# Optimization experiments

Hardware: AMD Instinct MI355X
Metric: run time of the kernel (lower is better)

## Reference

```python
import jax, jax.numpy as jnp
import numpy as np


def setup_inputs() -> dict:
    key = jax.random.key(0)
    k1, k2, k3 = jax.random.split(key, 3)
    B, T, J, D = 32, 1024, 256, 512
    context = jax.random.normal(k1, (B, T, D), dtype=jnp.float32)
    query = jax.random.normal(k2, (B, J, D), dtype=jnp.float32)
    # nn.Linear(3*D, 1, bias=False) weight, flattened to (3D,)
    w_alpha = jax.random.normal(k3, (3 * D,), dtype=jnp.float32) * (1.0 / np.sqrt(3 * D))
    return {"context": context, "query": query, "w_alpha": w_alpha}


def reference(context, query, w_alpha):
    # context: [B,T,D], query: [B,J,D], w_alpha: [3D]
    D = context.shape[-1]
    w1, w2, w3 = w_alpha[:D], w_alpha[D:2 * D], w_alpha[2 * D:]
    # Decomposed trilinear score: S[b,t,j] = c_t.w1 + q_j.w2 + sum_d c_td q_jd w3_d
    # (identical math to expand+concat+Linear, without the B*T*J*3D intermediate)
    S = (context @ w1)[:, :, None] \
        + (query @ w2)[:, None, :] \
        + jnp.einsum('btd,bjd->btj', context * w3, query)  # [B,T,J]
    S_softmax_row = jax.nn.softmax(S, axis=1)              # softmax over context dim (as in source)
    b_t = jax.nn.softmax(jnp.max(S, axis=2), axis=1)       # [B,T]
    U_attd = jnp.einsum('btj,bjd->btd', S_softmax_row, query)  # [B,T,D]
    h = jnp.einsum('bt,btd->bd', b_t, context)             # [B,D]
    H_attd = h[:, None, :]                                  # broadcast over T
    G = jnp.concatenate(
        [context, U_attd, context * U_attd, context * H_attd], axis=2)  # [B,T,4D]
    return G
```

## Files before the change

kernel.cpp:

```cpp
#include <hip/hip_runtime.h>
#include <cmath>

constexpr int B = 32, T = 1024, J = 256, D = 512;

typedef __attribute__((ext_vector_type(8))) short bf16x8;
typedef __attribute__((ext_vector_type(4))) float f32x4;
typedef __attribute__((ext_vector_type(8))) unsigned short u16x8;
typedef __attribute__((ext_vector_type(4))) unsigned short u16x4;
using u16 = unsigned short;

constexpr size_t OFF_S   = 0;
constexpr size_t OFF_CH  = OFF_S   + (size_t)B*T*J;
constexpr size_t OFF_CL  = OFF_CH  + (size_t)B*T*D/2;
constexpr size_t OFF_QPH = OFF_CL  + (size_t)B*T*D/2;
constexpr size_t OFF_QPL = OFF_QPH + (size_t)B*J*D/2;
constexpr size_t OFF_QTH = OFF_QPL + (size_t)B*J*D/2;
constexpr size_t OFF_QTL = OFF_QTH + (size_t)B*J*D/2;
constexpr size_t OFF_PH  = OFF_QTL + (size_t)B*J*D/2;
constexpr size_t OFF_PLO = OFF_PH  + (size_t)B*T*J/2;
constexpr size_t OFF_RT  = OFF_PLO + (size_t)B*T*J/2;
constexpr size_t OFF_CT  = OFF_RT  + (size_t)B*T;
constexpr size_t OFF_M   = OFF_CT  + (size_t)B*J;
constexpr size_t OFF_IL  = OFF_M   + (size_t)B*J;
constexpr size_t OFF_RM  = OFF_IL  + (size_t)B*J;
constexpr size_t OFF_BT  = OFF_RM  + (size_t)B*T;
constexpr size_t OFF_H   = OFF_BT  + (size_t)B*T;
constexpr size_t OFF_PM  = OFF_H   + (size_t)B*D;
constexpr size_t OFF_PL2 = OFF_PM  + (size_t)B*16*J;

__device__ __forceinline__ u16 f2bf(float x) {
  unsigned u = __float_as_uint(x);
  u += 0x7FFFu + ((u >> 16) & 1u);
  return (u16)(u >> 16);
}
__device__ __forceinline__ float bf2f(u16 h) {
  return __uint_as_float((unsigned)h << 16);
}

__global__ void k_prep_c(const float* __restrict__ ctx, const float* __restrict__ w_alpha,
                         float* __restrict__ rt, u16* __restrict__ ch, u16* __restrict__ cl) {
  int wid = threadIdx.x >> 6, lane = threadIdx.x & 63;
  size_t row = (size_t)blockIdx.x * 4 + wid;
  const float4* s4 = (const float4*)(ctx + row * D);
  const float4* w4 = (const float4*)w_alpha;
  float4 a0 = s4[lane*2], a1 = s4[lane*2+1];
  float4 b0 = w4[lane*2], b1 = w4[lane*2+1];
  float acc = a0.x*b0.x + a0.y*b0.y + a0.z*b0.z + a0.w*b0.w
            + a1.x*b1.x + a1.y*b1.y + a1.z*b1.z + a1.w*b1.w;
  float v[8] = {a0.x,a0.y,a0.z,a0.w,a1.x,a1.y,a1.z,a1.w};
  u16x8 hv, lv;
  #pragma unroll
  for (int i = 0; i < 8; ++i) {
    u16 hb = f2bf(v[i]);
    hv[i] = hb;
    lv[i] = f2bf(v[i] - bf2f(hb));
  }
  *(u16x8*)(ch + row*D + lane*8) = hv;
  *(u16x8*)(cl + row*D + lane*8) = lv;
  #pragma unroll
  for (int off = 32; off; off >>= 1) acc += __shfl_down(acc, off);
  if (lane == 0) rt[row] = acc;
}

__global__ void k_prep_q(const float* __restrict__ q, const float* __restrict__ w_alpha,
                         float* __restrict__ ct, u16* __restrict__ qph, u16* __restrict__ qpl) {
  int wid = threadIdx.x >> 6, lane = threadIdx.x & 63;
  size_t row = (size_t)blockIdx.x * 4 + wid;
  const float4* q4 = (const float4*)(q + row * D);
  const float4* w2 = (const float4*)(w_alpha + D);
  const float4* w3 = (const float4*)(w_alpha + 2 * D);
  float4 a0 = q4[lane*2], a1 = q4[lane*2+1];
  float4 b0 = w2[lane*2], b1 = w2[lane*2+1];
  float4 c0 = w3[lane*2], c1 = w3[lane*2+1];
  float acc = a0.x*b0.x + a0.y*b0.y + a0.z*b0.z + a0.w*b0.w
            + a1.x*b1.x + a1.y*b1.y + a1.z*b1.z + a1.w*b1.w;
  float v[8] = {a0.x*c0.x, a0.y*c0.y, a0.z*c0.z, a0.w*c0.w,
                a1.x*c1.x, a1.y*c1.y, a1.z*c1.z, a1.w*c1.w};
  u16x8 hv, lv;
  #pragma unroll
  for (int i = 0; i < 8; ++i) {
    u16 hb = f2bf(v[i]);
    hv[i] = hb;
    lv[i] = f2bf(v[i] - bf2f(hb));
  }
  *(u16x8*)(qph + row*D + lane*8) = hv;
  *(u16x8*)(qpl + row*D + lane*8) = lv;
  #pragma unroll
  for (int off = 32; off; off >>= 1) acc += __shfl_down(acc, off);
  if (lane == 0) ct[row] = acc;
}

__global__ void k_qt(const float* __restrict__ q, u16* __restrict__ qth, u16* __restrict__ qtl) {
  __shared__ float tl[64][65];
  int b = blockIdx.y;
  int j0 = (blockIdx.x & 3) * 64;
  int d0 = (blockIdx.x >> 2) * 64;
  int r = threadIdx.x >> 4, c = threadIdx.x & 15;
  #pragma unroll
  for (int rr = 0; rr < 4; ++rr) {
    int jl = r + rr*16;
    float4 v = *(const float4*)(q + ((size_t)b*J + j0 + jl)*D + d0 + c*4);
    tl[jl][c*4+0] = v.x; tl[jl][c*4+1] = v.y; tl[jl][c*4+2] = v.z; tl[jl][c*4+3] = v.w;
  }
  __syncthreads();
  #pragma unroll
  for (int rr = 0; rr < 4; ++rr) {
    int dl = r + rr*16;
    u16x4 hv, lv;
    #pragma unroll
    for (int k = 0; k < 4; ++k) {
      float v = tl[c*4+k][dl];
      u16 hb = f2bf(v);
      hv[k] = hb;
      lv[k] = f2bf(v - bf2f(hb));
    }
    size_t o = ((size_t)b*D + d0 + dl)*J + j0 + c*4;
    *(u16x4*)(qth + o) = hv;
    *(u16x4*)(qtl + o) = lv;
  }
}

struct FragSet { bf16x8 ah[4], al[4], bh[4], bl[4]; };

__device__ __forceinline__ void ld_frags(FragSet& f,
    const u16* __restrict__ Ah, const u16* __restrict__ Al,
    const u16* __restrict__ Bh, const u16* __restrict__ Bl,
    int ld, int k0) {
  #pragma unroll
  for (int i = 0; i < 4; ++i) {
    f.ah[i] = *(const bf16x8*)(Ah + (size_t)(i*16)*ld + k0);
    f.al[i] = *(const bf16x8*)(Al + (size_t)(i*16)*ld + k0);
    f.bh[i] = *(const bf16x8*)(Bh + (size_t)(i*16)*ld + k0);
    f.bl[i] = *(const bf16x8*)(Bl + (size_t)(i*16)*ld + k0);
  }
}

__device__ __forceinline__ void mm3(f32x4 acc[4][4], const FragSet& f) {
  #pragma unroll
  for (int i = 0; i < 4; ++i)
    #pragma unroll
    for (int j = 0; j < 4; ++j) {
      f32x4 a = acc[i][j];
      a = __builtin_amdgcn_mfma_f32_16x16x32_bf16(f.ah[i], f.bh[j], a, 0, 0, 0);
      a = __builtin_amdgcn_mfma_f32_16x16x32_bf16(f.ah[i], f.bl[j], a, 0, 0, 0);
      a = __builtin_amdgcn_mfma_f32_16x16x32_bf16(f.al[i], f.bh[j], a, 0, 0, 0);
      acc[i][j] = a;
    }
}

__global__ __launch_bounds__(256)
void k_sgemm_mfma(const u16* __restrict__ ch, const u16* __restrict__ cl,
                  const u16* __restrict__ qph, const u16* __restrict__ qpl,
                  const float* __restrict__ rt, const float* __restrict__ ct,
                  float* __restrict__ S, float* __restrict__ pm, float* __restrict__ pl,
                  float* __restrict__ rm) {
  __shared__ float rmx[4][64];
  const int b = blockIdx.y, mblk = blockIdx.x;
  const int m0 = mblk * 64;
  const int w = threadIdx.x >> 6, lane = threadIdx.x & 63;
  const int lr = lane & 15, lg = lane >> 4;
  const int n0 = w * 64;
  const u16* Ah = ch  + ((size_t)b*T + m0 + lr)*D + lg*8;
  const u16* Al = cl  + ((size_t)b*T + m0 + lr)*D + lg*8;
  const u16* Bh = qph + ((size_t)b*J + n0 + lr)*D + lg*8;
  const u16* Bl = qpl + ((size_t)b*J + n0 + lr)*D + lg*8;
  f32x4 acc[4][4];
  #pragma unroll
  for (int i = 0; i < 4; ++i)
    #pragma unroll
    for (int j = 0; j < 4; ++j) acc[i][j] = (f32x4){0.f, 0.f, 0.f, 0.f};
  FragSet f0, f1;
  ld_frags(f0, Ah, Al, Bh, Bl, D, 0);
  for (int k0 = 0; k0 < D; k0 += 64) {
    ld_frags(f1, Ah, Al, Bh, Bl, D, k0 + 32);
    mm3(acc, f0);
    int kn = (k0 + 64 < D) ? k0 + 64 : 0;
    ld_frags(f0, Ah, Al, Bh, Bl, D, kn);
    mm3(acc, f1);
  }
  #pragma unroll
  for (int mi = 0; mi < 4; ++mi) {
    float rv[4];
    #pragma unroll
    for (int r = 0; r < 4; ++r) rv[r] = rt[(size_t)b*T + m0 + mi*16 + lg*4 + r];
    #pragma unroll
    for (int nj = 0; nj < 4; ++nj) {
      float cv = ct[(size_t)b*J + n0 + nj*16 + lr];
      #pragma unroll
      for (int r = 0; r < 4; ++r) acc[mi][nj][r] += rv[r] + cv;
    }
  }
  float* Sb = S + (size_t)b*T*J;
  #pragma unroll
  for (int mi = 0; mi < 4; ++mi)
    #pragma unroll
    for (int r = 0; r < 4; ++r) {
      size_t ro = (size_t)(m0 + mi*16 + lg*4 + r) * J;
      #pragma unroll
      for (int nj = 0; nj < 4; ++nj)
        Sb[ro + n0 + nj*16 + lr] = acc[mi][nj][r];
    }
  #pragma unroll
  for (int nj = 0; nj < 4; ++nj) {
    float m = -INFINITY;
    #pragma unroll
    for (int mi = 0; mi < 4; ++mi)
      #pragma unroll
      for (int r = 0; r < 4; ++r) m = fmaxf(m, acc[mi][nj][r]);
    m = fmaxf(m, __shfl_xor(m, 16));
    m = fmaxf(m, __shfl_xor(m, 32));
    float s = 0.f;
    #pragma unroll
    for (int mi = 0; mi < 4; ++mi)
      #pragma unroll
      for (int r = 0; r < 4; ++r) s += __expf(acc[mi][nj][r] - m);
    s += __shfl_xor(s, 16);
    s += __shfl_xor(s, 32);
    if (lg == 0) {
      pm[((size_t)b*16 + mblk)*J + n0 + nj*16 + lr] = m;
      pl[((size_t)b*16 + mblk)*J + n0 + nj*16 + lr] = s;
    }
  }
  #pragma unroll
  for (int mi = 0; mi < 4; ++mi)
    #pragma unroll
    for (int r = 0; r < 4; ++r) {
      float m = -INFINITY;
      #pragma unroll
      for (int nj = 0; nj < 4; ++nj) m = fmaxf(m, acc[mi][nj][r]);
      m = fmaxf(m, __shfl_xor(m, 1));
      m = fmaxf(m, __shfl_xor(m, 2));
      m = fmaxf(m, __shfl_xor(m, 4));
      m = fmaxf(m, __shfl_xor(m, 8));
      if (lr == 0) rmx[w][mi*16 + lg*4 + r] = m;
    }
  __syncthreads();
  if (threadIdx.x < 64) {
    float m = fmaxf(fmaxf(rmx[0][threadIdx.x], rmx[1][threadIdx.x]),
                    fmaxf(rmx[2][threadIdx.x], rmx[3][threadIdx.x]));
    rm[(size_t)b*T + m0 + threadIdx.x] = m;
  }
}

__global__ void k_colcombine(const float* __restrict__ pm, const float* __restrict__ pl,
                             float* __restrict__ mcol, float* __restrict__ invl) {
  int b = blockIdx.x, j = threadIdx.x;
  float m = -INFINITY, l = 0.f;
  for (int c = 0; c < 16; ++c) {
    float pmv = pm[((size_t)b * 16 + c) * J + j];
    float plv = pl[((size_t)b * 16 + c) * J + j];
    float mn = fmaxf(m, pmv);
    l = l * __expf(m - mn) + plv * __expf(pmv - mn);
    m = mn;
  }
  mcol[b * J + j] = m;
  invl[b * J + j] = 1.f / l;
}

__global__ void k_btsm(const float* __restrict__ rm, float* __restrict__ bt) {
  __shared__ float red[4];
  int b = blockIdx.x, tid = threadIdx.x;
  int wid = tid >> 6, lane = tid & 63;
  float4 x = ((const float4*)(rm + (size_t)b * T))[tid];
  float m = fmaxf(fmaxf(x.x, x.y), fmaxf(x.z, x.w));
  #pragma unroll
  for (int off = 32; off; off >>= 1) m = fmaxf(m, __shfl_down(m, off));
  if (lane == 0) red[wid] = m;
  __syncthreads();
  float M = fmaxf(fmaxf(red[0], red[1]), fmaxf(red[2], red[3]));
  float e0 = __expf(x.x - M), e1 = __expf(x.y - M), e2 = __expf(x.z - M), e3 = __expf(x.w - M);
  float s = e0 + e1 + e2 + e3;
  #pragma unroll
  for (int off = 32; off; off >>= 1) s += __shfl_down(s, off);
  __syncthreads();
  if (lane == 0) red[wid] = s;
  __syncthreads();
  float inv = 1.f / (red[0] + red[1] + red[2] + red[3]);
  ((float4*)(bt + (size_t)b * T))[tid] = make_float4(e0 * inv, e1 * inv, e2 * inv, e3 * inv);
}

__global__ void k_h(const float* __restrict__ C, const float* __restrict__ bt,
                    float* __restrict__ h) {
  int b = blockIdx.y, chunk = blockIdx.x, tid = threadIdx.x;
  const float* Cb = C + (size_t)b * T * D + (size_t)chunk * 128 * D;
  const float* wb = bt + b * T + chunk * 128;
  float2 acc = make_float2(0.f, 0.f);
  for (int t = 0; t < 128; ++t) {
    float w = wb[t];
    float2 v = ((const float2*)(Cb + (size_t)t * D))[tid];
    acc.x = fmaf(w, v.x, acc.x);
    acc.y = fmaf(w, v.y, acc.y);
  }
  atomicAdd(&h[b * D + tid * 2],     acc.x);
  atomicAdd(&h[b * D + tid * 2 + 1], acc.y);
}

__global__ void k_pexp(const float* __restrict__ S, const float* __restrict__ mcol,
                       const float* __restrict__ invl,
                       u16* __restrict__ ph, u16* __restrict__ plo) {
  int wid = threadIdx.x >> 6, lane = threadIdx.x & 63;
  size_t row = (size_t)blockIdx.x * 4 + wid;
  int b = (int)(row >> 10);
  float4 s  = ((const float4*)(S + row * J))[lane];
  float4 mv = ((const float4*)(mcol + (size_t)b * J))[lane];
  float4 iv = ((const float4*)(invl + (size_t)b * J))[lane];
  float p[4] = {__expf(s.x - mv.x) * iv.x, __expf(s.y - mv.y) * iv.y,
                __expf(s.z - mv.z) * iv.z, __expf(s.w - mv.w) * iv.w};
  u16x4 hv, lv;
  #pragma unroll
  for (int i = 0; i < 4; ++i) {
    u16 hb = f2bf(p[i]);
    hv[i] = hb;
    lv[i] = f2bf(p[i] - bf2f(hb));
  }
  *(u16x4*)(ph  + row * J + lane * 4) = hv;
  *(u16x4*)(plo + row * J + lane * 4) = lv;
}

__global__ __launch_bounds__(256)
void k_umfma(const u16* __restrict__ ph, const u16* __restrict__ plo,
             const u16* __restrict__ qth, const u16* __restrict__ qtl,
             const float* __restrict__ ctx, const float* __restrict__ h,
             float* __restrict__ out) {
  const int b = blockIdx.y;
  const int mblk = blockIdx.x >> 1, nb = blockIdx.x & 1;
  const int m0 = mblk * 64;
  const int w = threadIdx.x >> 6, lane = threadIdx.x & 63;
  const int lr = lane & 15, lg = lane >> 4;
  const int n0 = nb * 256 + w * 64;
  const u16* Ahp = ph  + ((size_t)b*T + m0 + lr)*J + lg*8;
  const u16* Alp = plo + ((size_t)b*T + m0 + lr)*J + lg*8;
  const u16* Bhp = qth + ((size_t)b*D + n0 + lr)*J + lg*8;
  const u16* Blp = qtl + ((size_t)b*D + n0 + lr)*J + lg*8;
  f32x4 acc[4][4];
  #pragma unroll
  for (int i = 0; i < 4; ++i)
    #pragma unroll
    for (int j = 0; j < 4; ++j) acc[i][j] = (f32x4){0.f, 0.f, 0.f, 0.f};
  FragSet f0, f1;
  ld_frags(f0, Ahp, Alp, Bhp, Blp, J, 0);
  for (int k0 = 0; k0 < J; k0 += 64) {
    ld_frags(f1, Ahp, Alp, Bhp, Blp, J, k0 + 32);
    mm3(acc, f0);
    int kn = (k0 + 64 < J) ? k0 + 64 : 0;
    ld_frags(f0, Ahp, Alp, Bhp, Blp, J, kn);
    mm3(acc, f1);
  }
  float hv[4];
  #pragma unroll
  for (int nj = 0; nj < 4; ++nj) hv[nj] = h[(size_t)b*D + n0 + nj*16 + lr];
  const float* Cb = ctx + (size_t)b * T * D;
  float* ob = out + (size_t)b * T * (size_t)(4 * D);
  #pragma unroll
  for (int mi = 0; mi < 4; ++mi)
    #pragma unroll
    for (int r = 0; r < 4; ++r) {
      int t = m0 + mi*16 + lg*4 + r;
      const float* crow = Cb + (size_t)t * D;
      float* orow = ob + (size_t)t * 2048;
      #pragma unroll
      for (int nj = 0; nj < 4; ++nj) {
        int d = n0 + nj*16 + lr;
        float u = acc[mi][nj][r];
        float c = crow[d];
        orow[d]          = c;
        orow[512  + d]   = u;
        orow[1024 + d]   = c * u;
        orow[1536 + d]   = c * hv[nj];
      }
    }
}

extern "C" void kernel_launch(void* const* d_in, const int* in_sizes, int n_in,
                              void* d_out, int out_size, void* d_ws, size_t ws_size,
                              hipStream_t stream) {
  const float* context = (const float*)d_in[0];
  const float* query   = (const float*)d_in[1];
  const float* w_alpha = (const float*)d_in[2];
  float* out = (float*)d_out;
  float* ws  = (float*)d_ws;

  float* S    = ws + OFF_S;
  u16*   ch   = (u16*)(ws + OFF_CH);
  u16*   cl   = (u16*)(ws + OFF_CL);
  u16*   qph  = (u16*)(ws + OFF_QPH);
  u16*   qpl  = (u16*)(ws + OFF_QPL);
  u16*   qth  = (u16*)(ws + OFF_QTH);
  u16*   qtl  = (u16*)(ws + OFF_QTL);
  u16*   phb  = (u16*)(ws + OFF_PH);
  u16*   plb  = (u16*)(ws + OFF_PLO);
  float* rt   = ws + OFF_RT;
  float* ct   = ws + OFF_CT;
  float* mcol = ws + OFF_M;
  float* invl = ws + OFF_IL;
  float* rm   = ws + OFF_RM;
  float* bt   = ws + OFF_BT;
  float* h    = ws + OFF_H;
  float* pm   = ws + OFF_PM;
  float* pl2  = ws + OFF_PL2;

  hipMemsetAsync(h, 0, (size_t)B * D * sizeof(float), stream);

  k_prep_c<<<dim3(B * T / 4), 256, 0, stream>>>(context, w_alpha, rt, ch, cl);
  k_prep_q<<<dim3(B * J / 4), 256, 0, stream>>>(query, w_alpha, ct, qph, qpl);
  k_qt    <<<dim3(32, B), 256, 0, stream>>>(query, qth, qtl);
  k_sgemm_mfma<<<dim3(16, B), 256, 0, stream>>>(ch, cl, qph, qpl, rt, ct, S, pm, pl2, rm);
  k_colcombine<<<dim3(B), 256, 0, stream>>>(pm, pl2, mcol, invl);
  k_btsm  <<<dim3(B), 256, 0, stream>>>(rm, bt);
  k_h     <<<dim3(8, B), 256, 0, stream>>>(context, bt, h);
  k_pexp  <<<dim3(B * T / 4), 256, 0, stream>>>(S, mcol, invl, phb, plb);
  k_umfma <<<dim3(32, B), 256, 0, stream>>>(phb, plb, qth, qtl, context, h, out);
}
```

Baseline: 533.6 us.

## Fuse context split and softmax-exp into LDS-tiled MFMA GEMMs

Removes the standalone context bf16 split kernel and the P exponent/split kernel. Both conversions now happen inside the two GEMMs while tiles are staged into swizzled shared memory, and the row dot with w1 is computed on the fly. The GEMMs use larger 128x256 tiles with 512 threads, block-index remapping, and register prefetch, which cuts global traffic for the hi/lo intermediates and improves operand reuse. It also halves the column-partial count and doubles k_h's parallelism. The cost is more synchronisation, more LDS use, and redundant exp/convert work across the N-split blocks.

New measurement: 442.3 us. 17.1% less time.

```diff
diff --git a/kernel.cpp b/kernel.cpp
--- a/kernel.cpp
+++ b/kernel.cpp
@@ -10,23 +10,18 @@
 using u16 = unsigned short;
 
 constexpr size_t OFF_S   = 0;
-constexpr size_t OFF_CH  = OFF_S   + (size_t)B*T*J;
-constexpr size_t OFF_CL  = OFF_CH  + (size_t)B*T*D/2;
-constexpr size_t OFF_QPH = OFF_CL  + (size_t)B*T*D/2;
+constexpr size_t OFF_QPH = OFF_S   + (size_t)B*T*J;
 constexpr size_t OFF_QPL = OFF_QPH + (size_t)B*J*D/2;
 constexpr size_t OFF_QTH = OFF_QPL + (size_t)B*J*D/2;
 constexpr size_t OFF_QTL = OFF_QTH + (size_t)B*J*D/2;
-constexpr size_t OFF_PH  = OFF_QTL + (size_t)B*J*D/2;
-constexpr size_t OFF_PLO = OFF_PH  + (size_t)B*T*J/2;
-constexpr size_t OFF_RT  = OFF_PLO + (size_t)B*T*J/2;
-constexpr size_t OFF_CT  = OFF_RT  + (size_t)B*T;
+constexpr size_t OFF_CT  = OFF_QTL + (size_t)B*J*D/2;
 constexpr size_t OFF_M   = OFF_CT  + (size_t)B*J;
 constexpr size_t OFF_IL  = OFF_M   + (size_t)B*J;
 constexpr size_t OFF_RM  = OFF_IL  + (size_t)B*J;
 constexpr size_t OFF_BT  = OFF_RM  + (size_t)B*T;
 constexpr size_t OFF_H   = OFF_BT  + (size_t)B*T;
 constexpr size_t OFF_PM  = OFF_H   + (size_t)B*D;
-constexpr size_t OFF_PL2 = OFF_PM  + (size_t)B*16*J;
+constexpr size_t OFF_PL2 = OFF_PM  + (size_t)B*8*J;
 
 __device__ __forceinline__ u16 f2bf(float x) {
   unsigned u = __float_as_uint(x);
@@ -37,29 +32,23 @@
   return __uint_as_float((unsigned)h << 16);
 }
 
-__global__ void k_prep_c(const float* __restrict__ ctx, const float* __restrict__ w_alpha,
-                         float* __restrict__ rt, u16* __restrict__ ch, u16* __restrict__ cl) {
-  int wid = threadIdx.x >> 6, lane = threadIdx.x & 63;
-  size_t row = (size_t)blockIdx.x * 4 + wid;
-  const float4* s4 = (const float4*)(ctx + row * D);
-  const float4* w4 = (const float4*)w_alpha;
-  float4 a0 = s4[lane*2], a1 = s4[lane*2+1];
-  float4 b0 = w4[lane*2], b1 = w4[lane*2+1];
-  float acc = a0.x*b0.x + a0.y*b0.y + a0.z*b0.z + a0.w*b0.w
-            + a1.x*b1.x + a1.y*b1.y + a1.z*b1.z + a1.w*b1.w;
-  float v[8] = {a0.x,a0.y,a0.z,a0.w,a1.x,a1.y,a1.z,a1.w};
-  u16x8 hv, lv;
-  #pragma unroll
-  for (int i = 0; i < 8; ++i) {
-    u16 hb = f2bf(v[i]);
-    hv[i] = hb;
-    lv[i] = f2bf(v[i] - bf2f(hb));
-  }
-  *(u16x8*)(ch + row*D + lane*8) = hv;
-  *(u16x8*)(cl + row*D + lane*8) = lv;
-  #pragma unroll
-  for (int off = 32; off; off >>= 1) acc += __shfl_down(acc, off);
-  if (lane == 0) rt[row] = acc;
+__device__ __forceinline__ int swz(int row, int c) {
+  return row * 32 + ((c ^ ((row >> 1) & 3)) << 3);
+}
+
+__device__ __forceinline__ void mm3(f32x4 acc[4][4],
+    const bf16x8 ah[4], const bf16x8 al[4],
+    const bf16x8 bh[4], const bf16x8 bl[4]) {
+  #pragma unroll
+  for (int i = 0; i < 4; ++i)
+    #pragma unroll
+    for (int j = 0; j < 4; ++j) {
+      f32x4 a = acc[i][j];
+      a = __builtin_amdgcn_mfma_f32_16x16x32_bf16(ah[i], bh[j], a, 0, 0, 0);
+      a = __builtin_amdgcn_mfma_f32_16x16x32_bf16(ah[i], bl[j], a, 0, 0, 0);
+      a = __builtin_amdgcn_mfma_f32_16x16x32_bf16(al[i], bh[j], a, 0, 0, 0);
+      acc[i][j] = a;
+    }
 }
 
 __global__ void k_prep_q(const float* __restrict__ q, const float* __restrict__ w_alpha,
@@ -120,85 +109,109 @@
   }
 }
 
-struct FragSet { bf16x8 ah[4], al[4], bh[4], bl[4]; };
-
-__device__ __forceinline__ void ld_frags(FragSet& f,
-    const u16* __restrict__ Ah, const u16* __restrict__ Al,
-    const u16* __restrict__ Bh, const u16* __restrict__ Bl,
-    int ld, int k0) {
-  #pragma unroll
-  for (int i = 0; i < 4; ++i) {
-    f.ah[i] = *(const bf16x8*)(Ah + (size_t)(i*16)*ld + k0);
-    f.al[i] = *(const bf16x8*)(Al + (size_t)(i*16)*ld + k0);
-    f.bh[i] = *(const bf16x8*)(Bh + (size_t)(i*16)*ld + k0);
-    f.bl[i] = *(const bf16x8*)(Bl + (size_t)(i*16)*ld + k0);
-  }
-}
-
-__device__ __forceinline__ void mm3(f32x4 acc[4][4], const FragSet& f) {
+__global__ __launch_bounds__(512, 2)
+void k_sgemm2(const float* __restrict__ ctx, const u16* __restrict__ qph,
+              const u16* __restrict__ qpl, const float* __restrict__ w_alpha,
+              const float* __restrict__ ct, float* __restrict__ S,
+              float* __restrict__ pm, float* __restrict__ pl, float* __restrict__ rm) {
+  __shared__ __align__(16) u16 Ah[128*32], Al[128*32], Bh[256*32], Bl[256*32];
+  __shared__ float w1s[512];
+  __shared__ float rts[128];
+  __shared__ float pcm[2][256], pcl[2][256];
+  __shared__ float rmx[4][128];
+  const int bid = blockIdx.x;
+  const int wg = (bid & 7) * 32 + (bid >> 3);
+  const int b = wg >> 3, mblk = wg & 7;
+  const int m0 = mblk * 128;
+  const int tid = threadIdx.x;
+  const int lane = tid & 63, w = tid >> 6;
+  const int lr = lane & 15, lg = lane >> 4;
+  const int wr = w >> 2, wc = w & 3;
+  const int arow = tid >> 2, ac = tid & 3;
+  w1s[tid & 511] = w_alpha[tid & 511];
+  const float* Cb = ctx + ((size_t)b*T + m0) * D;
+  const u16* Bhg = qph + (size_t)b*J*D;
+  const u16* Blg = qpl + (size_t)b*J*D;
+  f32x4 acc[4][4];
   #pragma unroll
   for (int i = 0; i < 4; ++i)
     #pragma unroll
-    for (int j = 0; j < 4; ++j) {
-      f32x4 a = acc[i][j];
-      a = __builtin_amdgcn_mfma_f32_16x16x32_bf16(f.ah[i], f.bh[j], a, 0, 0, 0);
-      a = __builtin_amdgcn_mfma_f32_16x16x32_bf16(f.ah[i], f.bl[j], a, 0, 0, 0);
-      a = __builtin_amdgcn_mfma_f32_16x16x32_bf16(f.al[i], f.bh[j], a, 0, 0, 0);
-      acc[i][j] = a;
-    }
-}
-
-__global__ __launch_bounds__(256)
-void k_sgemm_mfma(const u16* __restrict__ ch, const u16* __restrict__ cl,
-                  const u16* __restrict__ qph, const u16* __restrict__ qpl,
-                  const float* __restrict__ rt, const float* __restrict__ ct,
-                  float* __restrict__ S, float* __restrict__ pm, float* __restrict__ pl,
-                  float* __restrict__ rm) {
-  __shared__ float rmx[4][64];
-  const int b = blockIdx.y, mblk = blockIdx.x;
-  const int m0 = mblk * 64;
-  const int w = threadIdx.x >> 6, lane = threadIdx.x & 63;
-  const int lr = lane & 15, lg = lane >> 4;
-  const int n0 = w * 64;
-  const u16* Ah = ch  + ((size_t)b*T + m0 + lr)*D + lg*8;
-  const u16* Al = cl  + ((size_t)b*T + m0 + lr)*D + lg*8;
-  const u16* Bh = qph + ((size_t)b*J + n0 + lr)*D + lg*8;
-  const u16* Bl = qpl + ((size_t)b*J + n0 + lr)*D + lg*8;
-  f32x4 acc[4][4];
-  #pragma unroll
-  for (int i = 0; i < 4; ++i)
-    #pragma unroll
     for (int j = 0; j < 4; ++j) acc[i][j] = (f32x4){0.f, 0.f, 0.f, 0.f};
-  FragSet f0, f1;
-  ld_frags(f0, Ah, Al, Bh, Bl, D, 0);
-  for (int k0 = 0; k0 < D; k0 += 64) {
-    ld_frags(f1, Ah, Al, Bh, Bl, D, k0 + 32);
-    mm3(acc, f0);
-    int kn = (k0 + 64 < D) ? k0 + 64 : 0;
-    ld_frags(f0, Ah, Al, Bh, Bl, D, kn);
-    mm3(acc, f1);
-  }
-  #pragma unroll
-  for (int mi = 0; mi < 4; ++mi) {
-    float rv[4];
-    #pragma unroll
-    for (int r = 0; r < 4; ++r) rv[r] = rt[(size_t)b*T + m0 + mi*16 + lg*4 + r];
-    #pragma unroll
-    for (int nj = 0; nj < 4; ++nj) {
-      float cv = ct[(size_t)b*J + n0 + nj*16 + lr];
-      #pragma unroll
-      for (int r = 0; r < 4; ++r) acc[mi][nj][r] += rv[r] + cv;
-    }
-  }
-  float* Sb = S + (size_t)b*T*J;
+  float rtacc = 0.f;
+  float4 a0, a1;
+  bf16x8 qh0, qh1, ql0, ql1;
+  a0 = *(const float4*)(Cb + (size_t)arow*D + ac*8);
+  a1 = *(const float4*)(Cb + (size_t)arow*D + ac*8 + 4);
+  qh0 = *(const bf16x8*)(Bhg + (size_t)arow*D + ac*8);
+  ql0 = *(const bf16x8*)(Blg + (size_t)arow*D + ac*8);
+  qh1 = *(const bf16x8*)(Bhg + (size_t)(arow+128)*D + ac*8);
+  ql1 = *(const bf16x8*)(Blg + (size_t)(arow+128)*D + ac*8);
+  __syncthreads();
+  for (int ks = 0; ks < 16; ++ks) {
+    __syncthreads();
+    float av[8] = {a0.x,a0.y,a0.z,a0.w,a1.x,a1.y,a1.z,a1.w};
+    u16x8 hh, ll;
+    #pragma unroll
+    for (int i = 0; i < 8; ++i) {
+      u16 hb = f2bf(av[i]);
+      hh[i] = hb;
+      ll[i] = f2bf(av[i] - bf2f(hb));
+    }
+    *(u16x8*)&Ah[swz(arow, ac)] = hh;
+    *(u16x8*)&Al[swz(arow, ac)] = ll;
+    *(bf16x8*)&Bh[swz(arow, ac)]     = qh0;
+    *(bf16x8*)&Bl[swz(arow, ac)]     = ql0;
+    *(bf16x8*)&Bh[swz(arow+128, ac)] = qh1;
+    *(bf16x8*)&Bl[swz(arow+128, ac)] = ql1;
+    const int kb = ks*32 + ac*8;
+    rtacc += av[0]*w1s[kb+0] + av[1]*w1s[kb+1] + av[2]*w1s[kb+2] + av[3]*w1s[kb+3]
+           + av[4]*w1s[kb+4] + av[5]*w1s[kb+5] + av[6]*w1s[kb+6] + av[7]*w1s[kb+7];
+    __syncthreads();
+    if (ks < 15) {
+      const int k0 = (ks + 1) * 32;
+      a0 = *(const float4*)(Cb + (size_t)arow*D + k0 + ac*8);
+      a1 = *(const float4*)(Cb + (size_t)arow*D + k0 + ac*8 + 4);
+      qh0 = *(const bf16x8*)(Bhg + (size_t)arow*D + k0 + ac*8);
+      ql0 = *(const bf16x8*)(Blg + (size_t)arow*D + k0 + ac*8);
+      qh1 = *(const bf16x8*)(Bhg + (size_t)(arow+128)*D + k0 + ac*8);
+      ql1 = *(const bf16x8*)(Blg + (size_t)(arow+128)*D + k0 + ac*8);
+    }
+    bf16x8 fah[4], fal[4], fbh[4], fbl[4];
+    #pragma unroll
+    for (int i = 0; i < 4; ++i) {
+      int ar = wr*64 + i*16 + lr;
+      int br = wc*64 + i*16 + lr;
+      fah[i] = *(const bf16x8*)&Ah[swz(ar, lg)];
+      fal[i] = *(const bf16x8*)&Al[swz(ar, lg)];
+      fbh[i] = *(const bf16x8*)&Bh[swz(br, lg)];
+      fbl[i] = *(const bf16x8*)&Bl[swz(br, lg)];
+    }
+    mm3(acc, fah, fal, fbh, fbl);
+  }
+  rtacc += __shfl_xor(rtacc, 1);
+  rtacc += __shfl_xor(rtacc, 2);
+  if ((lane & 3) == 0) rts[arow] = rtacc;
+  __syncthreads();
+  float cv[4];
+  #pragma unroll
+  for (int nj = 0; nj < 4; ++nj) cv[nj] = ct[(size_t)b*J + wc*64 + nj*16 + lr];
   #pragma unroll
   for (int mi = 0; mi < 4; ++mi)
     #pragma unroll
     for (int r = 0; r < 4; ++r) {
-      size_t ro = (size_t)(m0 + mi*16 + lg*4 + r) * J;
+      float rv = rts[wr*64 + mi*16 + lg*4 + r];
+      #pragma unroll
+      for (int nj = 0; nj < 4; ++nj) acc[mi][nj][r] += rv + cv[nj];
+    }
+  float* Sb = S + ((size_t)b*T + m0)*J;
+  #pragma unroll
+  for (int mi = 0; mi < 4; ++mi)
+    #pragma unroll
+    for (int r = 0; r < 4; ++r) {
+      size_t ro = (size_t)(wr*64 + mi*16 + lg*4 + r) * J;
       #pragma unroll
       for (int nj = 0; nj < 4; ++nj)
-        Sb[ro + n0 + nj*16 + lr] = acc[mi][nj][r];
+        Sb[ro + wc*64 + nj*16 + lr] = acc[mi][nj][r];
     }
   #pragma unroll
   for (int nj = 0; nj < 4; ++nj) {
@@ -217,8 +230,8 @@
     s += __shfl_xor(s, 16);
     s += __shfl_xor(s, 32);
     if (lg == 0) {
-      pm[((size_t)b*16 + mblk)*J + n0 + nj*16 + lr] = m;
-      pl[((size_t)b*16 + mblk)*J + n0 + nj*16 + lr] = s;
+      pcm[wr][wc*64 + nj*16 + lr] = m;
+      pcl[wr][wc*64 + nj*16 + lr] = s;
     }
   }
   #pragma unroll
@@ -232,13 +245,19 @@
       m = fmaxf(m, __shfl_xor(m, 2));
       m = fmaxf(m, __shfl_xor(m, 4));
       m = fmaxf(m, __shfl_xor(m, 8));
-      if (lr == 0) rmx[w][mi*16 + lg*4 + r] = m;
-    }
-  __syncthreads();
-  if (threadIdx.x < 64) {
-    float m = fmaxf(fmaxf(rmx[0][threadIdx.x], rmx[1][threadIdx.x]),
-                    fmaxf(rmx[2][threadIdx.x], rmx[3][threadIdx.x]));
-    rm[(size_t)b*T + m0 + threadIdx.x] = m;
+      if (lr == 0) rmx[wc][wr*64 + mi*16 + lg*4 + r] = m;
+    }
+  __syncthreads();
+  if (tid < 256) {
+    float m0v = pcm[0][tid], m1v = pcm[1][tid];
+    float mm = fmaxf(m0v, m1v);
+    float lsum = pcl[0][tid]*__expf(m0v - mm) + pcl[1][tid]*__expf(m1v - mm);
+    pm[((size_t)b*8 + mblk)*J + tid] = mm;
+    pl[((size_t)b*8 + mblk)*J + tid] = lsum;
+  } else if (tid < 384) {
+    int t = tid - 256;
+    float m = fmaxf(fmaxf(rmx[0][t], rmx[1][t]), fmaxf(rmx[2][t], rmx[3][t]));
+    rm[(size_t)b*T + m0 + t] = m;
   }
 }
 
@@ -246,9 +265,9 @@
                              float* __restrict__ mcol, float* __restrict__ invl) {
   int b = blockIdx.x, j = threadIdx.x;
   float m = -INFINITY, l = 0.f;
-  for (int c = 0; c < 16; ++c) {
-    float pmv = pm[((size_t)b * 16 + c) * J + j];
-    float plv = pl[((size_t)b * 16 + c) * J + j];
+  for (int c = 0; c < 8; ++c) {
+    float pmv = pm[((size_t)b * 8 + c) * J + j];
+    float plv = pl[((size_t)b * 8 + c) * J + j];
     float mn = fmaxf(m, pmv);
     l = l * __expf(m - mn) + plv * __expf(pmv - mn);
     m = mn;
@@ -282,10 +301,10 @@
 __global__ void k_h(const float* __restrict__ C, const float* __restrict__ bt,
                     float* __restrict__ h) {
   int b = blockIdx.y, chunk = blockIdx.x, tid = threadIdx.x;
-  const float* Cb = C + (size_t)b * T * D + (size_t)chunk * 128 * D;
-  const float* wb = bt + b * T + chunk * 128;
+  const float* Cb = C + (size_t)b * T * D + (size_t)chunk * 64 * D;
+  const float* wb = bt + b * T + chunk * 64;
   float2 acc = make_float2(0.f, 0.f);
-  for (int t = 0; t < 128; ++t) {
+  for (int t = 0; t < 64; ++t) {
     float w = wb[t];
     float2 v = ((const float2*)(Cb + (size_t)t * D))[tid];
     acc.x = fmaf(w, v.x, acc.x);
@@ -295,78 +314,105 @@
   atomicAdd(&h[b * D + tid * 2 + 1], acc.y);
 }
 
-__global__ void k_pexp(const float* __restrict__ S, const float* __restrict__ mcol,
-                       const float* __restrict__ invl,
-                       u16* __restrict__ ph, u16* __restrict__ plo) {
-  int wid = threadIdx.x >> 6, lane = threadIdx.x & 63;
-  size_t row = (size_t)blockIdx.x * 4 + wid;
-  int b = (int)(row >> 10);
-  float4 s  = ((const float4*)(S + row * J))[lane];
-  float4 mv = ((const float4*)(mcol + (size_t)b * J))[lane];
-  float4 iv = ((const float4*)(invl + (size_t)b * J))[lane];
-  float p[4] = {__expf(s.x - mv.x) * iv.x, __expf(s.y - mv.y) * iv.y,
-                __expf(s.z - mv.z) * iv.z, __expf(s.w - mv.w) * iv.w};
-  u16x4 hv, lv;
-  #pragma unroll
-  for (int i = 0; i < 4; ++i) {
-    u16 hb = f2bf(p[i]);
-    hv[i] = hb;
-    lv[i] = f2bf(p[i] - bf2f(hb));
-  }
-  *(u16x4*)(ph  + row * J + lane * 4) = hv;
-  *(u16x4*)(plo + row * J + lane * 4) = lv;
-}
-
-__global__ __launch_bounds__(256)
-void k_umfma(const u16* __restrict__ ph, const u16* __restrict__ plo,
-             const u16* __restrict__ qth, const u16* __restrict__ qtl,
-             const float* __restrict__ ctx, const float* __restrict__ h,
-             float* __restrict__ out) {
-  const int b = blockIdx.y;
-  const int mblk = blockIdx.x >> 1, nb = blockIdx.x & 1;
-  const int m0 = mblk * 64;
-  const int w = threadIdx.x >> 6, lane = threadIdx.x & 63;
+__global__ __launch_bounds__(512, 2)
+void k_umfma2(const float* __restrict__ S, const u16* __restrict__ qth,
+              const u16* __restrict__ qtl, const float* __restrict__ mcol,
+              const float* __restrict__ invl, const float* __restrict__ ctx,
+              const float* __restrict__ h, float* __restrict__ out) {
+  __shared__ __align__(16) u16 Ah[128*32], Al[128*32], Bh[256*32], Bl[256*32];
+  __shared__ float msl[256], isl[256];
+  const int bid = blockIdx.x;
+  const int wg = (bid & 7) * 64 + (bid >> 3);
+  const int b = wg >> 4, rest = wg & 15;
+  const int mblk = rest >> 1, nb = rest & 1;
+  const int m0 = mblk * 128, n0 = nb * 256;
+  const int tid = threadIdx.x;
+  const int lane = tid & 63, w = tid >> 6;
   const int lr = lane & 15, lg = lane >> 4;
-  const int n0 = nb * 256 + w * 64;
-  const u16* Ahp = ph  + ((size_t)b*T + m0 + lr)*J + lg*8;
-  const u16* Alp = plo + ((size_t)b*T + m0 + lr)*J + lg*8;
-  const u16* Bhp = qth + ((size_t)b*D + n0 + lr)*J + lg*8;
-  const u16* Blp = qtl + ((size_t)b*D + n0 + lr)*J + lg*8;
+  const int wr = w >> 2, wc = w & 3;
+  const int arow = tid >> 2, ac = tid & 3;
+  if (tid < 256) {
+    msl[tid] = mcol[(size_t)b*J + tid];
+    isl[tid] = invl[(size_t)b*J + tid];
+  }
+  const float* Sb = S + ((size_t)b*T + m0)*J;
+  const u16* Bhg = qth + ((size_t)b*D + n0)*J;
+  const u16* Blg = qtl + ((size_t)b*D + n0)*J;
   f32x4 acc[4][4];
   #pragma unroll
   for (int i = 0; i < 4; ++i)
     #pragma unroll
     for (int j = 0; j < 4; ++j) acc[i][j] = (f32x4){0.f, 0.f, 0.f, 0.f};
-  FragSet f0, f1;
-  ld_frags(f0, Ahp, Alp, Bhp, Blp, J, 0);
-  for (int k0 = 0; k0 < J; k0 += 64) {
-    ld_frags(f1, Ahp, Alp, Bhp, Blp, J, k0 + 32);
-    mm3(acc, f0);
-    int kn = (k0 + 64 < J) ? k0 + 64 : 0;
-    ld_frags(f0, Ahp, Alp, Bhp, Blp, J, kn);
-    mm3(acc, f1);
+  float4 a0, a1;
+  bf16x8 qh0, qh1, ql0, ql1;
+  a0 = *(const float4*)(Sb + (size_t)arow*J + ac*8);
+  a1 = *(const float4*)(Sb + (size_t)arow*J + ac*8 + 4);
+  qh0 = *(const bf16x8*)(Bhg + (size_t)arow*J + ac*8);
+  ql0 = *(const bf16x8*)(Blg + (size_t)arow*J + ac*8);
+  qh1 = *(const bf16x8*)(Bhg + (size_t)(arow+128)*J + ac*8);
+  ql1 = *(const bf16x8*)(Blg + (size_t)(arow+128)*J + ac*8);
+  __syncthreads();
+  for (int ks = 0; ks < 8; ++ks) {
+    __syncthreads();
+    float av[8] = {a0.x,a0.y,a0.z,a0.w,a1.x,a1.y,a1.z,a1.w};
+    const int jb = ks*32 + ac*8;
+    u16x8 hh, ll;
+    #pragma unroll
+    for (int i = 0; i < 8; ++i) {
+      float p = __expf(av[i] - msl[jb+i]) * isl[jb+i];
+      u16 hb = f2bf(p);
+      hh[i] = hb;
+      ll[i] = f2bf(p - bf2f(hb));
+    }
+    *(u16x8*)&Ah[swz(arow, ac)] = hh;
+    *(u16x8*)&Al[swz(arow, ac)] = ll;
+    *(bf16x8*)&Bh[swz(arow, ac)]     = qh0;
+    *(bf16x8*)&Bl[swz(arow, ac)]     = ql0;
+    *(bf16x8*)&Bh[swz(arow+128, ac)] = qh1;
+    *(bf16x8*)&Bl[swz(arow+128, ac)] = ql1;
+    __syncthreads();
+    if (ks < 7) {
+      const int k0 = (ks + 1) * 32;
+      a0 = *(const float4*)(Sb + (size_t)arow*J + k0 + ac*8);
+      a1 = *(const float4*)(Sb + (size_t)arow*J + k0 + ac*8 + 4);
+      qh0 = *(const bf16x8*)(Bhg + (size_t)arow*J + k0 + ac*8);
+      ql0 = *(const bf16x8*)(Blg + (size_t)arow*J + k0 + ac*8);
+      qh1 = *(const bf16x8*)(Bhg + (size_t)(arow+128)*J + k0 + ac*8);
+      ql1 = *(const bf16x8*)(Blg + (size_t)(arow+128)*J + k0 + ac*8);
+    }
+    bf16x8 fah[4], fal[4], fbh[4], fbl[4];
+    #pragma unroll
+    for (int i = 0; i < 4; ++i) {
+      int ar = wr*64 + i*16 + lr;
+      int br = wc*64 + i*16 + lr;
+      fah[i] = *(const bf16x8*)&Ah[swz(ar, lg)];
+      fal[i] = *(const bf16x8*)&Al[swz(ar, lg)];
+      fbh[i] = *(const bf16x8*)&Bh[swz(br, lg)];
+      fbl[i] = *(const bf16x8*)&Bl[swz(br, lg)];
+    }
+    mm3(acc, fah, fal, fbh, fbl);
   }
   float hv[4];
   #pragma unroll
-  for (int nj = 0; nj < 4; ++nj) hv[nj] = h[(size_t)b*D + n0 + nj*16 + lr];
-  const float* Cb = ctx + (size_t)b * T * D;
-  float* ob = out + (size_t)b * T * (size_t)(4 * D);
+  for (int nj = 0; nj < 4; ++nj) hv[nj] = h[(size_t)b*D + n0 + wc*64 + nj*16 + lr];
+  const float* Cb = ctx + ((size_t)b*T + m0) * D;
+  float* ob = out + ((size_t)b*T + m0) * 2048;
   #pragma unroll
   for (int mi = 0; mi < 4; ++mi)
     #pragma unroll
     for (int r = 0; r < 4; ++r) {
-      int t = m0 + mi*16 + lg*4 + r;
-      const float* crow = Cb + (size_t)t * D;
-      float* orow = ob + (size_t)t * 2048;
+      int trow = wr*64 + mi*16 + lg*4 + r;
+      const float* crow = Cb + (size_t)trow * D;
+      float* orow = ob + (size_t)trow * 2048;
       #pragma unroll
       for (int nj = 0; nj < 4; ++nj) {
-        int d = n0 + nj*16 + lr;
+        int d = n0 + wc*64 + nj*16 + lr;
         float u = acc[mi][nj][r];
         float c = crow[d];
-        orow[d]          = c;
-        orow[512  + d]   = u;
-        orow[1024 + d]   = c * u;
-        orow[1536 + d]   = c * hv[nj];
+        orow[d]        = c;
+        orow[512 + d]  = u;
+        orow[1024 + d] = c * u;
+        orow[1536 + d] = c * hv[nj];
       }
     }
 }
@@ -381,15 +427,10 @@
   float* ws  = (float*)d_ws;
 
   float* S    = ws + OFF_S;
-  u16*   ch   = (u16*)(ws + OFF_CH);
-  u16*   cl   = (u16*)(ws + OFF_CL);
   u16*   qph  = (u16*)(ws + OFF_QPH);
   u16*   qpl  = (u16*)(ws + OFF_QPL);
   u16*   qth  = (u16*)(ws + OFF_QTH);
   u16*   qtl  = (u16*)(ws + OFF_QTL);
-  u16*   phb  = (u16*)(ws + OFF_PH);
-  u16*   plb  = (u16*)(ws + OFF_PLO);
-  float* rt   = ws + OFF_RT;
   float* ct   = ws + OFF_CT;
   float* mcol = ws + OFF_M;
   float* invl = ws + OFF_IL;
@@ -401,13 +442,11 @@
 
   hipMemsetAsync(h, 0, (size_t)B * D * sizeof(float), stream);
 
-  k_prep_c<<<dim3(B * T / 4), 256, 0, stream>>>(context, w_alpha, rt, ch, cl);
   k_prep_q<<<dim3(B * J / 4), 256, 0, stream>>>(query, w_alpha, ct, qph, qpl);
   k_qt    <<<dim3(32, B), 256, 0, stream>>>(query, qth, qtl);
-  k_sgemm_mfma<<<dim3(16, B), 256, 0, stream>>>(ch, cl, qph, qpl, rt, ct, S, pm, pl2, rm);
+  k_sgemm2<<<dim3(256), 512, 0, stream>>>(context, qph, qpl, w_alpha, ct, S, pm, pl2, rm);
   k_colcombine<<<dim3(B), 256, 0, stream>>>(pm, pl2, mcol, invl);
   k_btsm  <<<dim3(B), 256, 0, stream>>>(rm, bt);
-  k_h     <<<dim3(8, B), 256, 0, stream>>>(context, bt, h);
-  k_pexp  <<<dim3(B * T / 4), 256, 0, stream>>>(S, mcol, invl, phb, plb);
-  k_umfma <<<dim3(32, B), 256, 0, stream>>>(phb, plb, qth, qtl, context, h, out);
-}
+  k_h     <<<dim3(16, B), 256, 0, stream>>>(context, bt, h);
+  k_umfma2<<<dim3(512), 512, 0, stream>>>(S, qth, qtl, mcol, invl, context, h, out);
+}
```
